# Optimization experiments

Measured on AMD Instinct MI355X. Metric: run time of the kernel, lower is better.

The kernel has to match this reference:

```python
import jax, jax.numpy as jnp
import numpy as np

B, S, D = 4, 8192, 1024

def log_g(x):
    # log of g(x): log(x + 0.5) for x >= 0, log(sigmoid(x)) = -softplus(-x) otherwise
    return jnp.where(x >= 0, jnp.log(jax.nn.relu(x) + 0.5), -jax.nn.softplus(-x))

def setup_inputs() -> dict:
    key = jax.random.key(0)
    k1, k2 = jax.random.split(key)
    x = jax.random.normal(k1, (B, S, D), dtype=jnp.float32)
    # Linear(dim, 3*dim, bias=False); stored as [dim, 3*dim] so y = x @ W
    W = jax.random.normal(k2, (D, 3 * D), dtype=jnp.float32) * (1.0 / np.sqrt(D))
    return {"x": x, "W": W}

def reference(x, W):
    # x: [B, S, D], W: [D, 3D]
    hW = jnp.einsum('bsd,de->bse', x, W)  # [B, S, 3D]
    hidden, f_gate, i_gate = jnp.split(hW, 3, axis=-1)

    # log-space normalized gates:
    # diff = softplus(-f) - softplus(-i); log_f' = -softplus(diff); log_i' = -softplus(-diff)
    diff = jax.nn.softplus(-f_gate) - jax.nn.softplus(-i_gate)
    log_f = -jax.nn.softplus(diff)
    log_i = -jax.nn.softplus(-diff)
    log_values = log_i + log_g(hidden)

    # Heinsen associative scan in log space (float32 internally)
    a_star = jnp.cumsum(log_f.astype(jnp.float32), axis=1)
    log_h0_plus_b_star = jax.lax.cumlogsumexp(log_values.astype(jnp.float32) - a_star, axis=1)
    log_h = a_star + log_h0_plus_b_star
    out = jnp.exp(log_h).astype(x.dtype)  # [B, S, D]
    return out
```

## Files before the change

### kernel.cpp

```cpp
#include <hip/hip_runtime.h>
#include <hip/hip_bf16.h>
#include <cstdint>
#include <cstddef>


#define BB 4
#define SS 8192
#define DD 1024
#define MM 32768
#define KK 1024
#define NN 3072
#define CHUNKS 512
#define CLEN 16
#define NCH 4096
#define NT 16

typedef __bf16 bf16;
typedef __bf16 bf16x2 __attribute__((ext_vector_type(2)));
typedef __bf16 bf16x4 __attribute__((ext_vector_type(4)));
typedef __bf16 bf16x8 __attribute__((ext_vector_type(8)));
typedef float f32x4 __attribute__((ext_vector_type(4)));

__device__ __forceinline__ void gload16(const bf16* g, bf16* l) {
  __builtin_amdgcn_global_load_lds(
      (const __attribute__((address_space(1))) unsigned int*)(const void*)g,
      (__attribute__((address_space(3))) unsigned int*)(void*)l,
      16, 0, 0);
}

__device__ __forceinline__ void gate2(float h, float f, float i,
                                      float& F, float& IG) {
  float P = __expf(fminf(-f, 80.f));
  float Q = __expf(fminf(-i, 80.f));
  float rZ = __builtin_amdgcn_rcpf(2.f + P + Q);
  float eh = __expf(fminf(-h, 80.f));
  float gh = (h >= 0.f) ? (h + 0.5f) : __builtin_amdgcn_rcpf(1.f + eh);
  F = (1.f + Q) * rZ;
  IG = (1.f + P) * gh * rZ;
}

__device__ __forceinline__ float laddexp(float a, float b) {
  float m = fmaxf(a, b);
  return m + __logf(1.f + __expf(fminf(a, b) - m));
}
__device__ __forceinline__ void comb(float& A, float& V, float Ac, float Vc) {
  V = laddexp(V + Ac, Vc);
  A += Ac;
}

__global__ __launch_bounds__(256) void k_cvt_x(const float4* __restrict__ x,
                                               bf16x4* __restrict__ xb) {
  int i = blockIdx.x * 256 + threadIdx.x;
  float4 v = x[i];
  bf16x4 o;
  o[0] = (bf16)v.x; o[1] = (bf16)v.y; o[2] = (bf16)v.z; o[3] = (bf16)v.w;
  xb[i] = o;
}

__global__ __launch_bounds__(256) void k_cvt_wt(const float* __restrict__ W,
                                                bf16* __restrict__ Wt) {
  __shared__ float tile[32][33];
  int n0 = blockIdx.x * 32, k0 = blockIdx.y * 32;
  int tx = threadIdx.x, ty = threadIdx.y;
#pragma unroll
  for (int i = 0; i < 32; i += 8)
    tile[ty + i][tx] = W[(size_t)(k0 + ty + i) * NN + n0 + tx];
  __syncthreads();
#pragma unroll
  for (int i = 0; i < 32; i += 8)
    Wt[(size_t)(n0 + ty + i) * KK + k0 + tx] = (bf16)tile[tx][ty + i];
}

__global__ __launch_bounds__(512, 2) void k_gemm(const bf16* __restrict__ A,
                                                 const bf16* __restrict__ Bt,
                                                 bf16* __restrict__ C) {
  __shared__ __align__(16) bf16 sm[65536];
  const int tid = threadIdx.x;
  const int lane = tid & 63;
  const int w = tid >> 6;
  const int wm = w >> 2;
  const int wn = w & 3;
  const int c16 = lane & 15;
  const int l4 = lane >> 4;

  int bid = blockIdx.x;
  int swz = (bid & 7) * 192 + (bid >> 3);
  int mT = swz / 12;
  int nT = swz - mT * 12;
  const int mBase = mT * 256, nBase = nT * 256;

  const int sr = tid >> 3;
  const int scol = ((tid & 7) ^ (sr & 7)) * 8;
  const bf16* gA = A + (size_t)(mBase + sr) * KK + scol;
  const bf16* gB = Bt + (size_t)(nBase + sr) * KK + scol;
  const int ld = tid * 8;

  const int sw8 = c16 & 7;
  const int sx0 = (l4 ^ sw8) * 8;
  const int sx1 = ((l4 + 4) ^ sw8) * 8;
  const int aRow = (wm * 64 + c16) * 64;
  const int bRow = (wn * 32 + c16) * 64;

  f32x4 acc[2][2][4][2];
#pragma unroll
  for (int a = 0; a < 2; ++a)
#pragma unroll
    for (int b2 = 0; b2 < 2; ++b2)
#pragma unroll
      for (int m = 0; m < 4; ++m)
#pragma unroll
        for (int n = 0; n < 2; ++n)
          acc[a][b2][m][n] = (f32x4){0.f, 0.f, 0.f, 0.f};

#define STGA(h, L, bo, ko) \
  gload16(gA + (h) * 131072 + (L) * 65536 + (ko), \
          sm + (bo) + (h) * 8192 + (L) * 4096 + ld)
#define STGB(h, L, bo, ko) \
  gload16(gB + (h) * 131072 + (L) * 65536 + (ko), \
          sm + (bo) + 16384 + (h) * 8192 + (L) * 4096 + ld)
#define LDA(qm, AF)                                                     \
  _Pragma("unroll") for (int mi = 0; mi < 4; ++mi) {                    \
    const bf16* p_ = sm + buf + (qm) * 8192 + aRow + mi * 1024;         \
    AF[mi][0] = *(const bf16x8*)(p_ + sx0);                             \
    AF[mi][1] = *(const bf16x8*)(p_ + sx1);                             \
  }
#define LDB(qn, BF)                                                     \
  _Pragma("unroll") for (int ni = 0; ni < 2; ++ni) {                    \
    const bf16* p_ = sm + buf + 16384 + (qn) * 8192 + bRow + ni * 1024; \
    BF[ni][0] = *(const bf16x8*)(p_ + sx0);                             \
    BF[ni][1] = *(const bf16x8*)(p_ + sx1);                             \
  }
#define MFMAQ(qm, qn, AF, BF)                                             \
  __builtin_amdgcn_s_setprio(1);                                          \
  _Pragma("unroll") for (int mi = 0; mi < 4; ++mi)                        \
  _Pragma("unroll") for (int ni = 0; ni < 2; ++ni) {                      \
    acc[qm][qn][mi][ni] = __builtin_amdgcn_mfma_f32_16x16x32_bf16(        \
        AF[mi][0], BF[ni][0], acc[qm][qn][mi][ni], 0, 0, 0);              \
    acc[qm][qn][mi][ni] = __builtin_amdgcn_mfma_f32_16x16x32_bf16(        \
        AF[mi][1], BF[ni][1], acc[qm][qn][mi][ni], 0, 0, 0);              \
  }                                                                       \
  __builtin_amdgcn_s_setprio(0);
#define BAR asm volatile("s_barrier" ::: "memory")
#define VMC(n) asm volatile("s_waitcnt vmcnt(" #n ")" ::: "memory")

  STGA(0, 0, 0, 0); STGA(0, 1, 0, 0); STGB(0, 0, 0, 0); STGB(0, 1, 0, 0);
  STGA(1, 0, 0, 0); STGA(1, 1, 0, 0); STGB(1, 0, 0, 0); STGB(1, 1, 0, 0);
  VMC(4);
  BAR;

  bf16x8 afr[4][2], bfr0[2][2], bfr1[2][2];

  for (int t = 0; t < NT - 1; ++t) {
    const int buf = (t & 1) << 15;
    const int nb = buf ^ 32768;
    const int ko = (t + 1) * 64;
    LDA(0, afr); LDB(0, bfr0);
    STGA(0, 0, nb, ko); STGA(0, 1, nb, ko);
    STGB(0, 0, nb, ko); STGB(0, 1, nb, ko);
    VMC(4);
    BAR;
    MFMAQ(0, 0, afr, bfr0);
    LDB(1, bfr1);
    STGA(1, 0, nb, ko); STGA(1, 1, nb, ko);
    MFMAQ(0, 1, afr, bfr1);
    LDA(1, afr);
    STGB(1, 0, nb, ko); STGB(1, 1, nb, ko);
    MFMAQ(1, 1, afr, bfr1);
    VMC(4);
    BAR;
    MFMAQ(1, 0, afr, bfr0);
  }
  {
    const int buf = 32768;
    LDA(0, afr); LDB(0, bfr0);
    VMC(0);
    BAR;
    MFMAQ(0, 0, afr, bfr0);
    LDB(1, bfr1);
    MFMAQ(0, 1, afr, bfr1);
    LDA(1, afr);
    MFMAQ(1, 1, afr, bfr1);
    MFMAQ(1, 0, afr, bfr0);
  }

  __syncthreads();
  const int rq = l4 * 4;
#pragma unroll
  for (int qm = 0; qm < 2; ++qm)
#pragma unroll
    for (int qn = 0; qn < 2; ++qn)
#pragma unroll
      for (int mi = 0; mi < 4; ++mi)
#pragma unroll
        for (int ni = 0; ni < 2; ++ni)
#pragma unroll
          for (int r = 0; r < 4; ++r) {
            int row = qm * 128 + wm * 64 + mi * 16 + rq + r;
            int col = (qn * 128 + wn * 32 + ni * 16 + c16) ^ ((row & 7) << 3);
            sm[row * 256 + col] = (bf16)acc[qm][qn][mi][ni][r];
          }
  __syncthreads();
#pragma unroll
  for (int p = 0; p < 16; ++p) {
    int row = p * 16 + (tid >> 5);
    int colL = (tid & 31) * 8;
    int col = colL ^ ((row & 7) << 3);
    bf16x8 v = *(const bf16x8*)(sm + row * 256 + col);
    *(bf16x8*)(C + (size_t)(mBase + row) * NN + nBase + colL) = v;
  }
#undef STGA
#undef STGB
#undef LDA
#undef LDB
#undef MFMAQ
#undef BAR
#undef VMC
}

__global__ __launch_bounds__(256, 6) void k_scan1(const bf16* __restrict__ hW,
                                                  float2* __restrict__ agg) {
  const int d0 = threadIdx.x * 4;
  const int b = blockIdx.y, c = blockIdx.z;
  const bf16* p = hW + (size_t)(b * SS + c * CLEN) * NN + d0;
  float Fp[4] = {1.f, 1.f, 1.f, 1.f};
  float v[4] = {0.f, 0.f, 0.f, 0.f};
  bf16x4 hh = *(const bf16x4*)(p);
  bf16x4 ff = *(const bf16x4*)(p + DD);
  bf16x4 ii = *(const bf16x4*)(p + 2 * DD);
#pragma unroll 4
  for (int j = 0; j < CLEN - 1; ++j) {
    p += NN;
    bf16x4 hn = *(const bf16x4*)(p);
    bf16x4 fn = *(const bf16x4*)(p + DD);
    bf16x4 in2 = *(const bf16x4*)(p + 2 * DD);
#pragma unroll
    for (int e = 0; e < 4; ++e) {
      float F, IG;
      gate2((float)hh[e], (float)ff[e], (float)ii[e], F, IG);
      v[e] = fmaf(v[e], F, IG);
      Fp[e] *= F;
    }
    hh = hn; ff = fn; ii = in2;
  }
#pragma unroll
  for (int e = 0; e < 4; ++e) {
    float F, IG;
    gate2((float)hh[e], (float)ff[e], (float)ii[e], F, IG);
    v[e] = fmaf(v[e], F, IG);
    Fp[e] *= F;
  }
  const size_t ch = (size_t)b * DD + d0;
#pragma unroll
  for (int e = 0; e < 4; ++e)
    agg[(ch + e) * CHUNKS + c] =
        make_float2(__logf(fmaxf(Fp[e], 1e-37f)), __logf(fmaxf(v[e], 1e-37f)));
}

__global__ __launch_bounds__(256) void k_scan2(const float2* __restrict__ agg,
                                               float2* __restrict__ pre) {
  const int ch = blockIdx.x * 4 + (threadIdx.x >> 6);
  const int lane = threadIdx.x & 63;
  const float4* src = (const float4*)(agg + (size_t)ch * CHUNKS);
  float4 v[4];
#pragma unroll
  for (int q = 0; q < 4; ++q) v[q] = src[lane * 4 + q];
  float A = v[0].x, V = v[0].y;
  comb(A, V, v[0].z, v[0].w);
#pragma unroll
  for (int q = 1; q < 4; ++q) {
    comb(A, V, v[q].x, v[q].y);
    comb(A, V, v[q].z, v[q].w);
  }
#pragma unroll
  for (int off = 1; off < 64; off <<= 1) {
    float Ao = __shfl_up(A, off);
    float Vo = __shfl_up(V, off);
    if (lane >= off) {
      V = laddexp(Vo + A, V);
      A = Ao + A;
    }
  }
  float exA = __shfl_up(A, 1);
  float exV = __shfl_up(V, 1);
  if (lane == 0) { exA = 0.f; exV = -1e30f; }
  float4* dst = (float4*)(pre + (size_t)ch * CHUNKS);
#pragma unroll
  for (int q = 0; q < 4; ++q) {
    float4 o;
    o.x = exA; o.y = exV;
    comb(exA, exV, v[q].x, v[q].y);
    o.z = exA; o.w = exV;
    comb(exA, exV, v[q].z, v[q].w);
    dst[lane * 4 + q] = o;
  }
}

__global__ __launch_bounds__(256, 6) void k_scan3(const bf16* __restrict__ hW,
                                                  const float2* __restrict__ pre,
                                                  float* __restrict__ out) {
  const int d0 = threadIdx.x * 4;
  const int b = blockIdx.y, c = blockIdx.z;
  const bf16* p = hW + (size_t)(b * SS + c * CLEN) * NN + d0;
  float* o = out + (size_t)(b * SS + c * CLEN) * DD + d0;
  const size_t ch = (size_t)b * DD + d0;
  float v[4];
#pragma unroll
  for (int e = 0; e < 4; ++e)
    v[e] = __expf(pre[(ch + e) * CHUNKS + c].y);
  bf16x4 hh = *(const bf16x4*)(p);
  bf16x4 ff = *(const bf16x4*)(p + DD);
  bf16x4 ii = *(const bf16x4*)(p + 2 * DD);
#pragma unroll 4
  for (int j = 0; j < CLEN - 1; ++j) {
    p += NN;
    bf16x4 hn = *(const bf16x4*)(p);
    bf16x4 fn = *(const bf16x4*)(p + DD);
    bf16x4 in2 = *(const bf16x4*)(p + 2 * DD);
    float4 ov;
#pragma unroll
    for (int e = 0; e < 4; ++e) {
      float F, IG;
      gate2((float)hh[e], (float)ff[e], (float)ii[e], F, IG);
      v[e] = fmaf(v[e], F, IG);
    }
    ov.x = v[0]; ov.y = v[1]; ov.z = v[2]; ov.w = v[3];
    *(float4*)o = ov;
    o += DD;
    hh = hn; ff = fn; ii = in2;
  }
  float4 ov;
#pragma unroll
  for (int e = 0; e < 4; ++e) {
    float F, IG;
    gate2((float)hh[e], (float)ff[e], (float)ii[e], F, IG);
    v[e] = fmaf(v[e], F, IG);
  }
  ov.x = v[0]; ov.y = v[1]; ov.z = v[2]; ov.w = v[3];
  *(float4*)o = ov;
}

extern "C" void kernel_launch(void* const* d_in, const int* in_sizes, int n_in,
                              void* d_out, int out_size, void* d_ws,
                              size_t ws_size, hipStream_t stream) {
  const float* x = (const float*)d_in[0];
  const float* W = (const float*)d_in[1];
  float* out = (float*)d_out;
  char* ws = (char*)d_ws;

  const size_t wtB = (size_t)NN * KK * 2;
  const size_t xbB = (size_t)MM * KK * 2;
  const size_t aggB = (size_t)CHUNKS * NCH * sizeof(float2);
  bf16* Wt = (bf16*)ws;
  bf16* xb = (bf16*)(ws + wtB);
  bf16* hW = (bf16*)(ws + wtB + xbB);
  float2* agg = (float2*)(ws + wtB);
  float2* pre = (float2*)(ws + wtB + aggB);

  k_cvt_wt<<<dim3(NN / 32, KK / 32), dim3(32, 8), 0, stream>>>(W, Wt);
  k_cvt_x<<<dim3(MM * KK / 4 / 256), dim3(256), 0, stream>>>((const float4*)x,
                                                             (bf16x4*)xb);
  k_gemm<<<dim3((NN / 256) * (MM / 256)), 512, 0, stream>>>(xb, Wt, hW);
  k_scan1<<<dim3(1, BB, CHUNKS), 256, 0, stream>>>(hW, agg);
  k_scan2<<<dim3(NCH / 4), 256, 0, stream>>>(agg, pre);
  k_scan3<<<dim3(1, BB, CHUNKS), 256, 0, stream>>>(hW, pre, out);
}
```

Before: 544.2 us.

## Transpose chunk aggregate layout, deepen scan prefetch, use exp2 in gates

The agg/pre aggregates move from a channel-major to a chunk-major layout, so k_scan1 and k_scan3 write and read contiguous float2 values across threads instead of strided ones. k_scan2 now does strided reads instead. The scan kernels are fully unrolled with a four-row-deep register prefetch, and the occupancy hint goes from 6 to 8. The gate math switches to exp2 with pre-scaled arguments. These aim to improve memory-level parallelism and coalescing, at the cost of register pressure and uncoalesced access in the small k_scan2 kernel.

New measurement: 528.8 us. -2.8%, faster.

```diff
diff --git a/kernel.cpp b/kernel.cpp
--- a/kernel.cpp
+++ b/kernel.cpp
@@ -28,13 +28,20 @@
       16, 0, 0);
 }
 
+#if __has_builtin(__builtin_amdgcn_exp2f)
+#define EXP2(x) __builtin_amdgcn_exp2f(x)
+#else
+#define EXP2(x) __expf((x) * 0.69314718056f)
+#endif
+
 __device__ __forceinline__ void gate2(float h, float f, float i,
                                       float& F, float& IG) {
-  float P = __expf(fminf(-f, 80.f));
-  float Q = __expf(fminf(-i, 80.f));
+  const float NL2E = -1.44269504089f;
+  float P = EXP2(fminf(f * NL2E, 60.f));
+  float Q = EXP2(fminf(i * NL2E, 60.f));
+  float H = EXP2(fminf(h * NL2E, 60.f));
   float rZ = __builtin_amdgcn_rcpf(2.f + P + Q);
-  float eh = __expf(fminf(-h, 80.f));
-  float gh = (h >= 0.f) ? (h + 0.5f) : __builtin_amdgcn_rcpf(1.f + eh);
+  float gh = (h >= 0.f) ? (h + 0.5f) : __builtin_amdgcn_rcpf(1.f + H);
   F = (1.f + Q) * rZ;
   IG = (1.f + P) * gh * rZ;
 }
@@ -217,42 +224,49 @@
 #undef VMC
 }
 
-__global__ __launch_bounds__(256, 6) void k_scan1(const bf16* __restrict__ hW,
+
+#define LDROW(s, pp)                      \
+  h##s = *(const bf16x4*)(pp);            \
+  f##s = *(const bf16x4*)((pp) + DD);     \
+  i##s = *(const bf16x4*)((pp) + 2 * DD)
+
+__global__ __launch_bounds__(256, 8) void k_scan1(const bf16* __restrict__ hW,
                                                   float2* __restrict__ agg) {
   const int d0 = threadIdx.x * 4;
   const int b = blockIdx.y, c = blockIdx.z;
   const bf16* p = hW + (size_t)(b * SS + c * CLEN) * NN + d0;
   float Fp[4] = {1.f, 1.f, 1.f, 1.f};
   float v[4] = {0.f, 0.f, 0.f, 0.f};
-  bf16x4 hh = *(const bf16x4*)(p);
-  bf16x4 ff = *(const bf16x4*)(p + DD);
-  bf16x4 ii = *(const bf16x4*)(p + 2 * DD);
-#pragma unroll 4
-  for (int j = 0; j < CLEN - 1; ++j) {
-    p += NN;
-    bf16x4 hn = *(const bf16x4*)(p);
-    bf16x4 fn = *(const bf16x4*)(p + DD);
-    bf16x4 in2 = *(const bf16x4*)(p + 2 * DD);
-#pragma unroll
-    for (int e = 0; e < 4; ++e) {
-      float F, IG;
-      gate2((float)hh[e], (float)ff[e], (float)ii[e], F, IG);
-      v[e] = fmaf(v[e], F, IG);
-      Fp[e] *= F;
-    }
-    hh = hn; ff = fn; ii = in2;
-  }
-#pragma unroll
-  for (int e = 0; e < 4; ++e) {
-    float F, IG;
-    gate2((float)hh[e], (float)ff[e], (float)ii[e], F, IG);
-    v[e] = fmaf(v[e], F, IG);
-    Fp[e] *= F;
-  }
-  const size_t ch = (size_t)b * DD + d0;
+  bf16x4 h0, f0, i0, h1, f1, i1, h2, f2, i2, h3, f3, i3;
+  LDROW(0, p); LDROW(1, p + NN); LDROW(2, p + 2 * NN); LDROW(3, p + 3 * NN);
+  const bf16* q = p + 4 * NN;
+#define C1(s)                                                         \
+  do {                                                                \
+    _Pragma("unroll") for (int e = 0; e < 4; ++e) {                   \
+      float F, IG;                                                    \
+      gate2((float)h##s[e], (float)f##s[e], (float)i##s[e], F, IG);   \
+      v[e] = fmaf(v[e], F, IG);                                       \
+      Fp[e] *= F;                                                     \
+    }                                                                 \
+  } while (0)
+  C1(0); LDROW(0, q); q += NN;
+  C1(1); LDROW(1, q); q += NN;
+  C1(2); LDROW(2, q); q += NN;
+  C1(3); LDROW(3, q); q += NN;
+  C1(0); LDROW(0, q); q += NN;
+  C1(1); LDROW(1, q); q += NN;
+  C1(2); LDROW(2, q); q += NN;
+  C1(3); LDROW(3, q); q += NN;
+  C1(0); LDROW(0, q); q += NN;
+  C1(1); LDROW(1, q); q += NN;
+  C1(2); LDROW(2, q); q += NN;
+  C1(3); LDROW(3, q);
+  C1(0); C1(1); C1(2); C1(3);
+#undef C1
+  float2* wout = agg + (size_t)c * NCH + b * DD + d0;
 #pragma unroll
   for (int e = 0; e < 4; ++e)
-    agg[(ch + e) * CHUNKS + c] =
+    wout[e] =
         make_float2(__logf(fmaxf(Fp[e], 1e-37f)), __logf(fmaxf(v[e], 1e-37f)));
 }
 
@@ -260,17 +274,13 @@
                                                float2* __restrict__ pre) {
   const int ch = blockIdx.x * 4 + (threadIdx.x >> 6);
   const int lane = threadIdx.x & 63;
-  const float4* src = (const float4*)(agg + (size_t)ch * CHUNKS);
-  float4 v[4];
-#pragma unroll
-  for (int q = 0; q < 4; ++q) v[q] = src[lane * 4 + q];
-  float A = v[0].x, V = v[0].y;
-  comb(A, V, v[0].z, v[0].w);
-#pragma unroll
-  for (int q = 1; q < 4; ++q) {
-    comb(A, V, v[q].x, v[q].y);
-    comb(A, V, v[q].z, v[q].w);
-  }
+  float2 vv[8];
+#pragma unroll
+  for (int q = 0; q < 8; ++q)
+    vv[q] = agg[(size_t)(lane * 8 + q) * NCH + ch];
+  float A = vv[0].x, V = vv[0].y;
+#pragma unroll
+  for (int q = 1; q < 8; ++q) comb(A, V, vv[q].x, vv[q].y);
 #pragma unroll
   for (int off = 1; off < 64; off <<= 1) {
     float Ao = __shfl_up(A, off);
@@ -283,60 +293,54 @@
   float exA = __shfl_up(A, 1);
   float exV = __shfl_up(V, 1);
   if (lane == 0) { exA = 0.f; exV = -1e30f; }
-  float4* dst = (float4*)(pre + (size_t)ch * CHUNKS);
-#pragma unroll
-  for (int q = 0; q < 4; ++q) {
-    float4 o;
-    o.x = exA; o.y = exV;
-    comb(exA, exV, v[q].x, v[q].y);
-    o.z = exA; o.w = exV;
-    comb(exA, exV, v[q].z, v[q].w);
-    dst[lane * 4 + q] = o;
-  }
-}
-
-__global__ __launch_bounds__(256, 6) void k_scan3(const bf16* __restrict__ hW,
+#pragma unroll
+  for (int q = 0; q < 8; ++q) {
+    pre[(size_t)(lane * 8 + q) * NCH + ch] = make_float2(exA, exV);
+    comb(exA, exV, vv[q].x, vv[q].y);
+  }
+}
+
+__global__ __launch_bounds__(256, 8) void k_scan3(const bf16* __restrict__ hW,
                                                   const float2* __restrict__ pre,
                                                   float* __restrict__ out) {
   const int d0 = threadIdx.x * 4;
   const int b = blockIdx.y, c = blockIdx.z;
   const bf16* p = hW + (size_t)(b * SS + c * CLEN) * NN + d0;
   float* o = out + (size_t)(b * SS + c * CLEN) * DD + d0;
-  const size_t ch = (size_t)b * DD + d0;
+  const float2* pr = pre + (size_t)c * NCH + b * DD + d0;
   float v[4];
 #pragma unroll
   for (int e = 0; e < 4; ++e)
-    v[e] = __expf(pre[(ch + e) * CHUNKS + c].y);
-  bf16x4 hh = *(const bf16x4*)(p);
-  bf16x4 ff = *(const bf16x4*)(p + DD);
-  bf16x4 ii = *(const bf16x4*)(p + 2 * DD);
-#pragma unroll 4
-  for (int j = 0; j < CLEN - 1; ++j) {
-    p += NN;
-    bf16x4 hn = *(const bf16x4*)(p);
-    bf16x4 fn = *(const bf16x4*)(p + DD);
-    bf16x4 in2 = *(const bf16x4*)(p + 2 * DD);
-    float4 ov;
-#pragma unroll
-    for (int e = 0; e < 4; ++e) {
-      float F, IG;
-      gate2((float)hh[e], (float)ff[e], (float)ii[e], F, IG);
-      v[e] = fmaf(v[e], F, IG);
-    }
-    ov.x = v[0]; ov.y = v[1]; ov.z = v[2]; ov.w = v[3];
-    *(float4*)o = ov;
-    o += DD;
-    hh = hn; ff = fn; ii = in2;
-  }
-  float4 ov;
-#pragma unroll
-  for (int e = 0; e < 4; ++e) {
-    float F, IG;
-    gate2((float)hh[e], (float)ff[e], (float)ii[e], F, IG);
-    v[e] = fmaf(v[e], F, IG);
-  }
-  ov.x = v[0]; ov.y = v[1]; ov.z = v[2]; ov.w = v[3];
-  *(float4*)o = ov;
+    v[e] = __expf(pr[e].y);
+  bf16x4 h0, f0, i0, h1, f1, i1, h2, f2, i2, h3, f3, i3;
+  LDROW(0, p); LDROW(1, p + NN); LDROW(2, p + 2 * NN); LDROW(3, p + 3 * NN);
+  const bf16* q = p + 4 * NN;
+#define C3(s)                                                         \
+  do {                                                                \
+    float4 ov;                                                        \
+    _Pragma("unroll") for (int e = 0; e < 4; ++e) {                   \
+      float F, IG;                                                    \
+      gate2((float)h##s[e], (float)f##s[e], (float)i##s[e], F, IG);   \
+      v[e] = fmaf(v[e], F, IG);                                       \
+    }                                                                 \
+    ov.x = v[0]; ov.y = v[1]; ov.z = v[2]; ov.w = v[3];               \
+    *(float4*)o = ov;                                                 \
+    o += DD;                                                          \
+  } while (0)
+  C3(0); LDROW(0, q); q += NN;
+  C3(1); LDROW(1, q); q += NN;
+  C3(2); LDROW(2, q); q += NN;
+  C3(3); LDROW(3, q); q += NN;
+  C3(0); LDROW(0, q); q += NN;
+  C3(1); LDROW(1, q); q += NN;
+  C3(2); LDROW(2, q); q += NN;
+  C3(3); LDROW(3, q); q += NN;
+  C3(0); LDROW(0, q); q += NN;
+  C3(1); LDROW(1, q); q += NN;
+  C3(2); LDROW(2, q); q += NN;
+  C3(3); LDROW(3, q);
+  C3(0); C3(1); C3(2); C3(3);
+#undef C3
 }
 
 extern "C" void kernel_launch(void* const* d_in, const int* in_sizes, int n_in,
```
